# Kernel tuning notes

Hardware: AMD Instinct MI355X
Metric: run time of the kernel (lower is better)

Reference implementation:

```python
import jax, jax.numpy as jnp
import numpy as np

N = 50000      # nodes
E = 800000     # edges
F_IN = 146
D = 256        # repr_len
H = 512        # GENConv hidden (expansion=2)
L = 25         # res blocks
EPS_MSG = 1e-7 # GENConv message eps
T = 0.01       # softmax aggregation temperature


def setup_inputs() -> dict:
    key = jax.random.key(0)
    ks = jax.random.split(key, 8)
    s = lambda k, shape, scale=0.05: jax.random.normal(k, shape, jnp.float32) * scale
    return dict(
        x=jax.random.uniform(ks[0], (N, F_IN), jnp.float32),
        edge_index=jax.random.randint(ks[1], (2, E), 0, N, jnp.int32),
        enc_W=s(ks[2], (F_IN, D)), enc_b=jnp.zeros((D,), jnp.float32),
        conv_W1=s(ks[3], (L, D, H)), conv_b1=jnp.zeros((L, H), jnp.float32),
        conv_ln_g=jnp.ones((L, H), jnp.float32), conv_ln_b=jnp.zeros((L, H), jnp.float32),
        conv_W2=s(ks[4], (L, H, D)), conv_b2=jnp.zeros((L, D), jnp.float32),
        res_ln_g=jnp.ones((L, D), jnp.float32), res_ln_b=jnp.zeros((L, D), jnp.float32),
        fc1_W=s(ks[5], (D, D // 2)), fc1_b=jnp.zeros((D // 2,), jnp.float32),
        out_W=s(ks[6], (D // 2, 1)), out_b=jnp.zeros((1,), jnp.float32),
    )


def layer_norm(x, g, b, eps=1e-5):
    mu = x.mean(-1, keepdims=True)
    var = ((x - mu) ** 2).mean(-1, keepdims=True)
    return (x - mu) * jax.lax.rsqrt(var + eps) * g + b


def genconv(x, src, dst, W1, b1, g1, bb1, W2, b2):
    # message: relu(x_j) + eps  (no edge_attr)
    msg = jax.nn.relu(x[src]) + EPS_MSG                    # [E, D]
    logit = msg * T
    m = jax.ops.segment_max(logit, dst, num_segments=N)    # per-dst, per-feature max
    m = jnp.where(jnp.isfinite(m), m, 0.0)                 # isolated nodes -> 0
    num = jnp.exp(logit - m[dst])
    den = jax.ops.segment_sum(num, dst, num_segments=N)
    alpha = num / (den[dst] + 1e-16)
    agg = jax.ops.segment_sum(alpha * msg, dst, num_segments=N)  # [N, D]
    h = agg + x                                            # root residual inside GENConv
    h = jax.nn.relu(layer_norm(h @ W1 + b1, g1, bb1))      # MLP: Lin->LN->ReLU->Lin
    return h @ W2 + b2


def reference(x, edge_index, enc_W, enc_b, conv_W1, conv_b1, conv_ln_g, conv_ln_b,
              conv_W2, conv_b2, res_ln_g, res_ln_b, fc1_W, fc1_b, out_W, out_b):
    src, dst = edge_index[0], edge_index[1]
    x = x.at[:, 121:].set(x[:, 121:] / 100.0 - 0.5)
    h = x @ enc_W + enc_b
    # layer 0: conv only
    h = genconv(h, src, dst, conv_W1[0], conv_b1[0], conv_ln_g[0], conv_ln_b[0],
                conv_W2[0], conv_b2[0])

    # layers 1..24: res+ block  (dropout=0.1 is identity in eval mode)
    def step(h, p):
        W1, b1, g1, bb1, W2, b2, rg, rb = p
        z = jax.nn.relu(layer_norm(h, rg, rb))
        z = genconv(z, src, dst, W1, b1, g1, bb1, W2, b2)
        return h + z, None

    params = (conv_W1[1:], conv_b1[1:], conv_ln_g[1:], conv_ln_b[1:],
              conv_W2[1:], conv_b2[1:], res_ln_g[1:], res_ln_b[1:])
    h, _ = jax.lax.scan(step, h, params)

    # final: layers[0].act(layers[0].norm(x))
    h = jax.nn.relu(layer_norm(h, res_ln_g[0], res_ln_b[0]))
    h = jax.nn.relu(h @ fc1_W + fc1_b)
    return h @ out_W + out_b
```

## Files before the change

### kernel.cpp

```cpp
#include <hip/hip_runtime.h>

#define NN 50000
#define NE 800000
#define FIN 146
#define DD 256
#define HHD 512
#define NL 25
#define MT 196
#define MT3 782
#define SCAN_NB 49

#define SWZ(r) (((r) >> 1) & 3)

typedef _Float16 h8 __attribute__((ext_vector_type(8)));
typedef float f32x4 __attribute__((ext_vector_type(4)));
typedef unsigned short us8 __attribute__((ext_vector_type(8)));
typedef _Float16 hf4 __attribute__((ext_vector_type(4)));

__device__ __forceinline__ float wsum(float v) {
#pragma unroll
  for (int off = 32; off > 0; off >>= 1) v += __shfl_xor(v, off, 64);
  return v;
}

__device__ __forceinline__ unsigned short f16b(float x) {
  _Float16 h = (_Float16)x;
  return __builtin_bit_cast(unsigned short, h);
}
__device__ __forceinline__ float f16f(unsigned short b) {
  return (float)__builtin_bit_cast(_Float16, b);
}

__device__ __forceinline__ void gl_lds16(const void* g, void* l) {
  __builtin_amdgcn_global_load_lds(
      (const __attribute__((address_space(1))) unsigned int*)g,
      (__attribute__((address_space(3))) unsigned int*)l, 16, 0, 0);
}

__global__ void count_k(const int* __restrict__ ei, int* __restrict__ deg) {
  int e = blockIdx.x * 256 + threadIdx.x;
  if (e < NE) atomicAdd(&deg[ei[NE + e]], 1);
}

__global__ __launch_bounds__(1024) void scan1_k(const int* __restrict__ deg,
                                                int* __restrict__ rp,
                                                int* __restrict__ bsum) {
  __shared__ int buf[1024];
  int tid = threadIdx.x, blk = blockIdx.x;
  int i = blk * 1024 + tid;
  buf[tid] = (i < NN) ? deg[i] : 0;
  __syncthreads();
#pragma unroll
  for (int off = 1; off < 1024; off <<= 1) {
    int t = (tid >= off) ? buf[tid - off] : 0;
    __syncthreads();
    buf[tid] += t;
    __syncthreads();
  }
  if (i < NN) rp[i + 1] = buf[tid];
  if (tid == 1023) bsum[blk] = buf[1023];
}

__global__ void scan2_k(int* __restrict__ bsum) {
  int tid = threadIdx.x;
  int v = (tid < SCAN_NB) ? bsum[tid] : 0;
#pragma unroll
  for (int off = 1; off < 64; off <<= 1) {
    int t = __shfl_up(v, off, 64);
    if (tid >= off) v += t;
  }
  if (tid < SCAN_NB) bsum[tid] = v;
}

__global__ __launch_bounds__(1024) void scan3_k(const int* __restrict__ bsum,
                                                int* __restrict__ rp,
                                                int* __restrict__ deg) {
  int i = blockIdx.x * 1024 + threadIdx.x;
  if (i < NN) {
    int blk = i >> 10;
    if (blk > 0) rp[i + 1] += bsum[blk - 1];
    deg[i] = 0;
  }
  if (i == 0) rp[0] = 0;
}

__global__ void fill_k(const int* __restrict__ ei, const int* __restrict__ rp,
                       int* __restrict__ deg, int* __restrict__ col) {
  int e = blockIdx.x * 256 + threadIdx.x;
  if (e < NE) {
    int d = ei[NE + e];
    int pos = rp[d] + atomicAdd(&deg[d], 1);
    col[pos] = ei[e];
  }
}

__global__ __launch_bounds__(256) void wconv_k(const float* __restrict__ cW1,
                                               const float* __restrict__ cW2,
                                               const float* __restrict__ fcW,
                                               const float* __restrict__ encW,
                                               unsigned short* __restrict__ wbuf,
                                               unsigned short* __restrict__ fc1t,
                                               unsigned short* __restrict__ encT) {
  int z = blockIdx.z;
  const float* W;
  unsigned short* oh;
  int Ksrc, Kpad, N;
  if (z < 50) {
    int l = z >> 1, which = z & 1;
    if (which == 0) { W = cW1 + (size_t)l * 131072; Ksrc = 256; N = 512; oh = wbuf + (size_t)l * 524288; }
    else            { W = cW2 + (size_t)l * 131072; Ksrc = 512; N = 256; oh = wbuf + (size_t)l * 524288 + 262144; }
    Kpad = Ksrc;
  } else if (z == 50) {
    W = fcW; Ksrc = 256; Kpad = 256; N = 128; oh = fc1t;
  } else {
    W = encW; Ksrc = FIN; Kpad = 160; N = 256; oh = encT;
  }
  if ((int)blockIdx.x >= (Kpad >> 5) || (int)blockIdx.y >= (N >> 5)) return;
  __shared__ float tile[32][33];
  int tx = threadIdx.x, ty = threadIdx.y;
  int k0 = blockIdx.x * 32, n0 = blockIdx.y * 32;
#pragma unroll
  for (int i = 0; i < 4; ++i) {
    int r = ty + i * 8;
    int k = k0 + r;
    tile[r][tx] = (k < Ksrc) ? W[(size_t)k * N + n0 + tx] : 0.f;
  }
  __syncthreads();
#pragma unroll
  for (int i = 0; i < 4; ++i) {
    int r = ty + i * 8;
    float v = tile[tx][r];
    oh[(size_t)(n0 + r) * Kpad + k0 + tx] = f16b(v);
  }
}

__global__ __launch_bounds__(256) void agg16_k(const hf4* __restrict__ z16,
                                               const int* __restrict__ rp,
                                               const int* __restrict__ col,
                                               unsigned short* __restrict__ hh16) {
  int node = blockIdx.x * 4 + (threadIdx.x >> 6);
  int lane = threadIdx.x & 63;
  if (node >= NN) return;
  int beg = rp[node], end = rp[node + 1];
  float4 s = make_float4(0.f, 0.f, 0.f, 0.f);
  float4 v = make_float4(0.f, 0.f, 0.f, 0.f);
  int j = beg;
  for (; j + 3 < end; j += 4) {
    int sn0 = col[j], sn1 = col[j + 1], sn2 = col[j + 2], sn3 = col[j + 3];
    hf4 a0 = z16[(size_t)sn0 * 64 + lane];
    hf4 a1 = z16[(size_t)sn1 * 64 + lane];
    hf4 a2 = z16[(size_t)sn2 * 64 + lane];
    hf4 a3 = z16[(size_t)sn3 * 64 + lane];
#pragma unroll
    for (int u = 0; u < 4; ++u) {
      hf4 a = (u == 0) ? a0 : (u == 1) ? a1 : (u == 2) ? a2 : a3;
      float m0 = fmaxf((float)a[0], 0.f) + 1e-7f;
      float m1 = fmaxf((float)a[1], 0.f) + 1e-7f;
      float m2 = fmaxf((float)a[2], 0.f) + 1e-7f;
      float m3 = fmaxf((float)a[3], 0.f) + 1e-7f;
      float e0 = __expf(m0 * 0.01f), e1 = __expf(m1 * 0.01f);
      float e2 = __expf(m2 * 0.01f), e3 = __expf(m3 * 0.01f);
      s.x += e0; s.y += e1; s.z += e2; s.w += e3;
      v.x = fmaf(e0, m0, v.x); v.y = fmaf(e1, m1, v.y);
      v.z = fmaf(e2, m2, v.z); v.w = fmaf(e3, m3, v.w);
    }
  }
  for (; j < end; ++j) {
    int sn = col[j];
    hf4 a = z16[(size_t)sn * 64 + lane];
    float m0 = fmaxf((float)a[0], 0.f) + 1e-7f;
    float m1 = fmaxf((float)a[1], 0.f) + 1e-7f;
    float m2 = fmaxf((float)a[2], 0.f) + 1e-7f;
    float m3 = fmaxf((float)a[3], 0.f) + 1e-7f;
    float e0 = __expf(m0 * 0.01f), e1 = __expf(m1 * 0.01f);
    float e2 = __expf(m2 * 0.01f), e3 = __expf(m3 * 0.01f);
    s.x += e0; s.y += e1; s.z += e2; s.w += e3;
    v.x = fmaf(e0, m0, v.x); v.y = fmaf(e1, m1, v.y);
    v.z = fmaf(e2, m2, v.z); v.w = fmaf(e3, m3, v.w);
  }
  hf4 ow = z16[(size_t)node * 64 + lane];
  float o0 = v.x / (s.x + 1e-16f) + (float)ow[0];
  float o1 = v.y / (s.y + 1e-16f) + (float)ow[1];
  float o2 = v.z / (s.z + 1e-16f) + (float)ow[2];
  float o3 = v.w / (s.w + 1e-16f) + (float)ow[3];
  size_t idx = (size_t)node * DD + lane * 4;
  *(ushort4*)&hh16[idx] = make_ushort4(f16b(o0), f16b(o1), f16b(o2), f16b(o3));
}

template <int AMODE, int ACC, int RELU, int PSUM, int C16, int Z16>
__global__ __launch_bounds__(512, 3) void mgemm_k(
    const float* __restrict__ Af, const unsigned short* __restrict__ A16,
    const unsigned short* __restrict__ BTh,
    const float* __restrict__ bias, float* __restrict__ C, int M, int K, int N,
    int mtiles, int lgnb,
    const float2* __restrict__ stats,
    const float* __restrict__ lng, const float* __restrict__ lnbeta,
    float2* __restrict__ psum_out, unsigned short* __restrict__ z16out) {
  __shared__ __align__(16) unsigned short Ash[2][8192], Bsh[2][4096];
  int tid = threadIdx.x;
  int bi = blockIdx.x;
  int ppx = (mtiles + 7) >> 3;
  int slot = bi >> 3;
  int panel = (bi & 7) * ppx + (slot >> lgnb);
  if (panel >= mtiles) return;
  int nblk = slot & ((1 << lgnb) - 1);
  int bm0 = panel * 256, bn0 = nblk * 128;
  int lane = tid & 63, wv = tid >> 6;
  int wr = (wv >> 1) * 64, wc = (wv & 1) * 64;
  int lr = lane & 15, lc = lane >> 4;
  f32x4 acc[4][4];
  f32x4 zf = {0.f, 0.f, 0.f, 0.f};
#pragma unroll
  for (int mi = 0; mi < 4; ++mi)
#pragma unroll
    for (int ni = 0; ni < 4; ++ni) acc[mi][ni] = zf;

  int sr = tid >> 1, hf = tid & 1;
  int arow = bm0 + sr;

  float mu = 0.f, rstd = 1.f;
  if constexpr (AMODE == 3) {
    if (arow < M) {
      float2 st = stats[arow];
      mu = st.x; rstd = st.y;
    }
  }

  auto stageB = [&](int buf, int k0) {
    int r = tid >> 2, cp = tid & 3;
    int c = cp ^ SWZ(r);
    gl_lds16(BTh + (size_t)(bn0 + r) * K + k0 + c * 8, &Bsh[buf][wv * 512]);
  };
  auto stageA = [&](int buf, int k0) {
    if constexpr (AMODE == 0) {
#pragma unroll
      for (int j = 0; j < 2; ++j) {
        int idx = wv * 128 + j * 64 + lane;
        int r = idx >> 2, cp = idx & 3;
        int c = cp ^ SWZ(r);
        int row = bm0 + r;
        if (row >= M) row = M - 1;
        gl_lds16(A16 + (size_t)row * K + k0 + c * 8, &Ash[buf][wv * 1024 + j * 512]);
      }
    } else {
      float v[16];
      if (arow < M) {
        if constexpr (AMODE == 2) {
          const float* xp = Af + (size_t)arow * FIN;
#pragma unroll
          for (int j = 0; j < 16; ++j) {
            int kk = k0 + hf * 16 + j;
            float t = (kk < FIN) ? xp[kk] : 0.f;
            if (kk >= 121 && kk < FIN) t = t * 0.01f - 0.5f;
            v[j] = t;
          }
        } else {
          const unsigned short* ap = A16 + (size_t)arow * K + k0 + hf * 16;
          us8 p0 = *(const us8*)(ap);
          us8 p1 = *(const us8*)(ap + 8);
          const float* gp = lng + k0 + hf * 16;
          const float* bp = lnbeta + k0 + hf * 16;
#pragma unroll
          for (int j = 0; j < 8; ++j) {
            v[j] = fmaxf(0.f, (f16f(p0[j]) - mu) * rstd * gp[j] + bp[j]);
            v[8 + j] = fmaxf(0.f, (f16f(p1[j]) - mu) * rstd * gp[8 + j] + bp[8 + j]);
          }
        }
      } else {
#pragma unroll
        for (int j = 0; j < 16; ++j) v[j] = 0.f;
      }
      unsigned short hi[16];
#pragma unroll
      for (int j = 0; j < 16; ++j) hi[j] = f16b(v[j]);
      int c0 = hf * 2;
      *(us8*)&Ash[buf][sr * 32 + ((c0 ^ SWZ(sr)) * 8)] = *(us8*)&hi[0];
      *(us8*)&Ash[buf][sr * 32 + (((c0 + 1) ^ SWZ(sr)) * 8)] = *(us8*)&hi[8];
    }
  };

  int nt = K / 32;
  stageA(0, 0);
  stageB(0, 0);
  __syncthreads();
  for (int t = 0; t < nt; ++t) {
    int cur = t & 1;
    h8 a[4], bh[4];
#pragma unroll
    for (int mi = 0; mi < 4; ++mi) {
      int r = wr + mi * 16 + lr;
      a[mi] = *(const h8*)&Ash[cur][r * 32 + ((lc ^ SWZ(r)) * 8)];
    }
#pragma unroll
    for (int ni = 0; ni < 4; ++ni) {
      int n = wc + ni * 16 + lr;
      bh[ni] = *(const h8*)&Bsh[cur][n * 32 + ((lc ^ SWZ(n)) * 8)];
    }
    if (t + 1 < nt) {
      stageA(cur ^ 1, (t + 1) * 32);
      stageB(cur ^ 1, (t + 1) * 32);
    }
    __builtin_amdgcn_s_setprio(1);
#pragma unroll
    for (int mi = 0; mi < 4; ++mi)
#pragma unroll
      for (int ni = 0; ni < 4; ++ni)
        acc[mi][ni] = __builtin_amdgcn_mfma_f32_16x16x32_f16(a[mi], bh[ni], acc[mi][ni], 0, 0, 0);
    __builtin_amdgcn_s_setprio(0);
    __syncthreads();
  }
  float sloc[16], qloc[16];
  if constexpr (PSUM) {
#pragma unroll
    for (int i = 0; i < 16; ++i) { sloc[i] = 0.f; qloc[i] = 0.f; }
  }
#pragma unroll
  for (int ni = 0; ni < 4; ++ni) {
    int colg = bn0 + wc + ni * 16 + lr;
    float bia = bias[colg];
#pragma unroll
    for (int mi = 0; mi < 4; ++mi) {
#pragma unroll
      for (int r = 0; r < 4; ++r) {
        int row = bm0 + wr + mi * 16 + lc * 4 + r;
        if (row < M) {
          float vv = acc[mi][ni][r] + bia;
          if (ACC) vv += C[(size_t)row * N + colg];
          if (RELU) vv = fmaxf(vv, 0.f);
          if constexpr (C16) {
            ((unsigned short*)C)[(size_t)row * N + colg] = f16b(vv);
          } else {
            C[(size_t)row * N + colg] = vv;
          }
          if constexpr (Z16) {
            z16out[(size_t)row * N + colg] = f16b(vv);
          }
          if constexpr (PSUM) {
            sloc[mi * 4 + r] += vv;
            qloc[mi * 4 + r] = fmaf(vv, vv, qloc[mi * 4 + r]);
          }
        }
      }
    }
  }
  if constexpr (PSUM) {
#pragma unroll
    for (int i = 0; i < 16; ++i) {
      float s = sloc[i], q = qloc[i];
#pragma unroll
      for (int off = 1; off < 16; off <<= 1) {
        s += __shfl_xor(s, off, 64);
        q += __shfl_xor(q, off, 64);
      }
      sloc[i] = s; qloc[i] = q;
    }
    __syncthreads();
    float2* lps = (float2*)&Ash[0][0];
    if (wv & 1) {
      if (lr == 0) {
#pragma unroll
        for (int mi = 0; mi < 4; ++mi)
#pragma unroll
          for (int r = 0; r < 4; ++r)
            lps[(wv >> 1) * 64 + mi * 16 + lc * 4 + r] =
                make_float2(sloc[mi * 4 + r], qloc[mi * 4 + r]);
      }
    }
    __syncthreads();
    if (!(wv & 1)) {
      if (lr == 0) {
#pragma unroll
        for (int mi = 0; mi < 4; ++mi)
#pragma unroll
          for (int r = 0; r < 4; ++r) {
            int rl = mi * 16 + lc * 4 + r;
            float2 o = lps[(wv >> 1) * 64 + rl];
            int row = bm0 + wr + rl;
            if (row < M)
              psum_out[(size_t)row * 4 + nblk] =
                  make_float2(sloc[mi * 4 + r] + o.x, qloc[mi * 4 + r] + o.y);
          }
      }
    }
  }
}

template <int ACC, int LAST>
__global__ __launch_bounds__(512, 3) void mgemm2_k(
    const unsigned short* __restrict__ A16,
    const unsigned short* __restrict__ BTh,
    const float* __restrict__ bias, unsigned short* __restrict__ h16,
    const float2* __restrict__ psum_in,
    const float* __restrict__ lng, const float* __restrict__ lnbeta,
    const float* __restrict__ rg, const float* __restrict__ rb,
    unsigned short* __restrict__ z16o, float2* __restrict__ hstats) {
  __shared__ __align__(16) unsigned short Ash[2][2048], Bsh[2][8192];
  const int M = NN, K = HHD, N = DD;
  int tid = threadIdx.x;
  int bi = blockIdx.x;
  int panel = (bi & 7) * 98 + (bi >> 3);
  if (panel >= MT3) return;
  int bm0 = panel * 64;
  int lane = tid & 63, wv = tid >> 6;
  int wr = (wv >> 2) * 32, wc = (wv & 3) * 64;
  int lr = lane & 15, lc = lane >> 4;
  f32x4 acc[2][4];
  f32x4 zf = {0.f, 0.f, 0.f, 0.f};
#pragma unroll
  for (int mi = 0; mi < 2; ++mi)
#pragma unroll
    for (int ni = 0; ni < 4; ++ni) acc[mi][ni] = zf;

  int sr2 = tid >> 2, q = tid & 3;
  int arow = bm0 + sr2;
  float mu = 0.f, rstd = 1.f;
  if (tid < 256 && arow < M) {
    float2 p0 = psum_in[(size_t)arow * 4 + 0];
    float2 p1 = psum_in[(size_t)arow * 4 + 1];
    float2 p2 = psum_in[(size_t)arow * 4 + 2];
    float2 p3 = psum_in[(size_t)arow * 4 + 3];
    float s = p0.x + p1.x + p2.x + p3.x;
    float qq = p0.y + p1.y + p2.y + p3.y;
    mu = s * (1.0f / HHD);
    float var = qq * (1.0f / HHD) - mu * mu;
    rstd = rsqrtf(var + 1e-5f);
  }

  auto stageB = [&](int buf, int k0) {
#pragma unroll
    for (int j = 0; j < 2; ++j) {
      int idx = j * 512 + tid;
      int r = idx >> 2, cp = idx & 3;
      int c = cp ^ SWZ(r);
      gl_lds16(BTh + (size_t)r * K + k0 + c * 8, &Bsh[buf][(j * 512 + wv * 64) * 8]);
    }
  };
  auto stageA = [&](int buf, int k0) {
    if (tid < 256) {
      float v[8];
      if (arow < M) {
        us8 p0 = *(const us8*)(A16 + (size_t)arow * K + k0 + q * 8);
        const float* gp = lng + k0 + q * 8;
        const float* bp = lnbeta + k0 + q * 8;
#pragma unroll
        for (int j = 0; j < 8; ++j)
          v[j] = fmaxf(0.f, (f16f(p0[j]) - mu) * rstd * gp[j] + bp[j]);
      } else {
#pragma unroll
        for (int j = 0; j < 8; ++j) v[j] = 0.f;
      }
      unsigned short hi[8];
#pragma unroll
      for (int j = 0; j < 8; ++j) hi[j] = f16b(v[j]);
      *(us8*)&Ash[buf][sr2 * 32 + ((q ^ SWZ(sr2)) * 8)] = *(us8*)&hi[0];
    }
  };

  const int nt = HHD / 32;
  stageA(0, 0);
  stageB(0, 0);
  __syncthreads();
  for (int t = 0; t < nt; ++t) {
    int cur = t & 1;
    h8 a[2], bh[4];
#pragma unroll
    for (int mi = 0; mi < 2; ++mi) {
      int r = wr + mi * 16 + lr;
      a[mi] = *(const h8*)&Ash[cur][r * 32 + ((lc ^ SWZ(r)) * 8)];
    }
#pragma unroll
    for (int ni = 0; ni < 4; ++ni) {
      int n = wc + ni * 16 + lr;
      bh[ni] = *(const h8*)&Bsh[cur][n * 32 + ((lc ^ SWZ(n)) * 8)];
    }
    if (t + 1 < nt) {
      stageA(cur ^ 1, (t + 1) * 32);
      stageB(cur ^ 1, (t + 1) * 32);
    }
    __builtin_amdgcn_s_setprio(1);
#pragma unroll
    for (int mi = 0; mi < 2; ++mi)
#pragma unroll
      for (int ni = 0; ni < 4; ++ni)
        acc[mi][ni] = __builtin_amdgcn_mfma_f32_16x16x32_f16(a[mi], bh[ni], acc[mi][ni], 0, 0, 0);
    __builtin_amdgcn_s_setprio(0);
    __syncthreads();
  }
  float sloc[8], qloc[8];
#pragma unroll
  for (int i = 0; i < 8; ++i) { sloc[i] = 0.f; qloc[i] = 0.f; }
#pragma unroll
  for (int ni = 0; ni < 4; ++ni) {
    int colg = wc + ni * 16 + lr;
    float bia = bias[colg];
#pragma unroll
    for (int mi = 0; mi < 2; ++mi) {
#pragma unroll
      for (int r = 0; r < 4; ++r) {
        int row = bm0 + wr + mi * 16 + lc * 4 + r;
        float vv = acc[mi][ni][r] + bia;
        if (row < M) {
          if (ACC) vv += f16f(h16[(size_t)row * N + colg]);
          h16[(size_t)row * N + colg] = f16b(vv);
        }
        acc[mi][ni][r] = vv;
        sloc[mi * 4 + r] += vv;
        qloc[mi * 4 + r] = fmaf(vv, vv, qloc[mi * 4 + r]);
      }
    }
  }
#pragma unroll
  for (int i = 0; i < 8; ++i) {
    float s = sloc[i], qq = qloc[i];
#pragma unroll
    for (int off = 1; off < 16; off <<= 1) {
      s += __shfl_xor(s, off, 64);
      qq += __shfl_xor(qq, off, 64);
    }
    sloc[i] = s; qloc[i] = qq;
  }
  __syncthreads();
  float2* lpart = (float2*)&Bsh[0][0];
  float2* rowst = (float2*)&Bsh[1][0];
  if (lr == 0) {
#pragma unroll
    for (int mi = 0; mi < 2; ++mi)
#pragma unroll
      for (int r = 0; r < 4; ++r) {
        int rl = wr + mi * 16 + lc * 4 + r;
        lpart[rl * 4 + (wv & 3)] = make_float2(sloc[mi * 4 + r], qloc[mi * 4 + r]);
      }
  }
  __syncthreads();
  if (tid < 64) {
    float2 p0 = lpart[tid * 4 + 0];
    float2 p1 = lpart[tid * 4 + 1];
    float2 p2 = lpart[tid * 4 + 2];
    float2 p3 = lpart[tid * 4 + 3];
    float s = p0.x + p1.x + p2.x + p3.x;
    float qq = p0.y + p1.y + p2.y + p3.y;
    float m_ = s * (1.0f / DD);
    float var = qq * (1.0f / DD) - m_ * m_;
    float rs = rsqrtf(var + 1e-5f);
    rowst[tid] = make_float2(m_, rs);
    if (LAST) {
      int row = bm0 + tid;
      if (row < M) hstats[row] = make_float2(m_, rs);
    }
  }
  __syncthreads();
  if (!LAST) {
#pragma unroll
    for (int mi = 0; mi < 2; ++mi) {
#pragma unroll
      for (int r = 0; r < 4; ++r) {
        int rl = wr + mi * 16 + lc * 4 + r;
        int row = bm0 + rl;
        if (row < M) {
          float2 st = rowst[rl];
#pragma unroll
          for (int ni = 0; ni < 4; ++ni) {
            int colg = wc + ni * 16 + lr;
            float z = fmaxf(0.f, (acc[mi][ni][r] - st.x) * st.y * rg[colg] + rb[colg]);
            z16o[(size_t)row * N + colg] = f16b(z);
          }
        }
      }
    }
  }
}

__global__ __launch_bounds__(256) void outmv_k(const float* __restrict__ t1,
                                               const float* __restrict__ oW,
                                               const float* __restrict__ ob,
                                               float* __restrict__ out) {
  int row = blockIdx.x * 4 + (threadIdx.x >> 6);
  int lane = threadIdx.x & 63;
  if (row >= NN) return;
  float2 v = *(const float2*)(t1 + (size_t)row * 128 + lane * 2);
  float2 w = *(const float2*)(oW + lane * 2);
  float s = v.x * w.x + v.y * w.y;
  s = wsum(s);
  if (lane == 0) out[row] = s + ob[0];
}

extern "C" void kernel_launch(void* const* d_in, const int* in_sizes, int n_in,
                              void* d_out, int out_size, void* d_ws, size_t ws_size,
                              hipStream_t stream) {
  const float* x = (const float*)d_in[0];
  const int* ei = (const int*)d_in[1];
  const float* encW = (const float*)d_in[2];
  const float* encb = (const float*)d_in[3];
  const float* cW1 = (const float*)d_in[4];
  const float* cb1 = (const float*)d_in[5];
  const float* clg = (const float*)d_in[6];
  const float* clb = (const float*)d_in[7];
  const float* cW2 = (const float*)d_in[8];
  const float* cb2 = (const float*)d_in[9];
  const float* rlg = (const float*)d_in[10];
  const float* rlb = (const float*)d_in[11];
  const float* fcW = (const float*)d_in[12];
  const float* fcb = (const float*)d_in[13];
  const float* oW = (const float*)d_in[14];
  const float* ob = (const float*)d_in[15];
  float* out = (float*)d_out;

  char* w = (char*)d_ws;
  unsigned short* h16 = (unsigned short*)(w);
  unsigned short* mid16 = (unsigned short*)(w + 51200000);
  float* t1 = (float*)(w + 51200000);
  hf4* z16 = (hf4*)(w + 102400000);
  unsigned short* hh16 = (unsigned short*)(w + 128000000);
  float2* psum = (float2*)(w + 153600000);
  float2* hstats = (float2*)(w + 155200000);
  int* rp = (int*)(w + 155600000);
  int* deg = (int*)(w + 155800064);
  int* col = (int*)(w + 156000128);
  unsigned short* wbuf = (unsigned short*)(w + 159200128);
  unsigned short* fc1t = (unsigned short*)(w + 185414528);
  unsigned short* encT = (unsigned short*)(w + 185545600);
  int* bsum = (int*)(w + 185709664);

  hipMemsetAsync(deg, 0, NN * sizeof(int), stream);
  count_k<<<(NE + 255) / 256, 256, 0, stream>>>(ei, deg);
  scan1_k<<<SCAN_NB, 1024, 0, stream>>>(deg, rp, bsum);
  scan2_k<<<1, 64, 0, stream>>>(bsum);
  scan3_k<<<SCAN_NB, 1024, 0, stream>>>(bsum, rp, deg);
  fill_k<<<(NE + 255) / 256, 256, 0, stream>>>(ei, rp, deg, col);

  wconv_k<<<dim3(16, 16, 52), dim3(32, 8), 0, stream>>>(cW1, cW2, fcW, encW, wbuf, fc1t, encT);

  mgemm_k<2, 0, 0, 0, 1, 0><<<400, 512, 0, stream>>>(
      x, nullptr, encT, encb, (float*)h16, NN, 160, DD, MT, 1,
      nullptr, nullptr, nullptr, nullptr, nullptr);

  for (int l = 0; l < NL; ++l) {
    const hf4* zsrc = (l == 0) ? (const hf4*)h16 : z16;
    agg16_k<<<NN / 4, 256, 0, stream>>>(zsrc, rp, col, hh16);

    const unsigned short* w1h = wbuf + (size_t)l * 524288;
    mgemm_k<0, 0, 0, 1, 1, 0><<<800, 512, 0, stream>>>(
        nullptr, hh16, w1h, cb1 + (size_t)l * HHD, (float*)mid16,
        NN, DD, HHD, MT, 2, nullptr, nullptr, nullptr, psum, nullptr);

    const unsigned short* w2h = wbuf + (size_t)l * 524288 + 262144;
    const float* lg = clg + (size_t)l * HHD;
    const float* lb = clb + (size_t)l * HHD;
    if (l == 0) {
      mgemm2_k<0, 0><<<784, 512, 0, stream>>>(
          mid16, w2h, cb2 + (size_t)l * DD, h16, psum, lg, lb,
          rlg + (size_t)(l + 1) * DD, rlb + (size_t)(l + 1) * DD,
          (unsigned short*)z16, nullptr);
    } else if (l < NL - 1) {
      mgemm2_k<1, 0><<<784, 512, 0, stream>>>(
          mid16, w2h, cb2 + (size_t)l * DD, h16, psum, lg, lb,
          rlg + (size_t)(l + 1) * DD, rlb + (size_t)(l + 1) * DD,
          (unsigned short*)z16, nullptr);
    } else {
      mgemm2_k<1, 1><<<784, 512, 0, stream>>>(
          mid16, w2h, cb2 + (size_t)l * DD, h16, psum, lg, lb,
          rlg, rlb, (unsigned short*)z16, hstats);
    }
  }

  mgemm_k<3, 0, 1, 0, 0, 0><<<200, 512, 0, stream>>>(
      nullptr, h16, fc1t, fcb, t1, NN, DD, 128, MT, 0,
      hstats, rlg, rlb, nullptr, nullptr);
  outmv_k<<<NN / 4, 256, 0, stream>>>(t1, oW, ob, out);
}
```

Measured before the change: 4.353 ms.

## Add dedicated 128x128-tile GEMM1 kernel and polynomial exp in aggregation

```diff
diff --git a/kernel.cpp b/kernel.cpp
--- a/kernel.cpp
+++ b/kernel.cpp
@@ -7,6 +7,7 @@
 #define HHD 512
 #define NL 25
 #define MT 196
+#define MT2 391
 #define MT3 782
 #define SCAN_NB 49
 
@@ -29,6 +30,10 @@
 }
 __device__ __forceinline__ float f16f(unsigned short b) {
   return (float)__builtin_bit_cast(_Float16, b);
+}
+
+__device__ __forceinline__ float exp_small(float x) {
+  return fmaf(x, fmaf(x, fmaf(x, 0.16666667f, 0.5f), 1.0f), 1.0f);
 }
 
 __device__ __forceinline__ void gl_lds16(const void* g, void* l) {
@@ -158,8 +163,8 @@
       float m1 = fmaxf((float)a[1], 0.f) + 1e-7f;
       float m2 = fmaxf((float)a[2], 0.f) + 1e-7f;
       float m3 = fmaxf((float)a[3], 0.f) + 1e-7f;
-      float e0 = __expf(m0 * 0.01f), e1 = __expf(m1 * 0.01f);
-      float e2 = __expf(m2 * 0.01f), e3 = __expf(m3 * 0.01f);
+      float e0 = exp_small(m0 * 0.01f), e1 = exp_small(m1 * 0.01f);
+      float e2 = exp_small(m2 * 0.01f), e3 = exp_small(m3 * 0.01f);
       s.x += e0; s.y += e1; s.z += e2; s.w += e3;
       v.x = fmaf(e0, m0, v.x); v.y = fmaf(e1, m1, v.y);
       v.z = fmaf(e2, m2, v.z); v.w = fmaf(e3, m3, v.w);
@@ -172,8 +177,8 @@
     float m1 = fmaxf((float)a[1], 0.f) + 1e-7f;
     float m2 = fmaxf((float)a[2], 0.f) + 1e-7f;
     float m3 = fmaxf((float)a[3], 0.f) + 1e-7f;
-    float e0 = __expf(m0 * 0.01f), e1 = __expf(m1 * 0.01f);
-    float e2 = __expf(m2 * 0.01f), e3 = __expf(m3 * 0.01f);
+    float e0 = exp_small(m0 * 0.01f), e1 = exp_small(m1 * 0.01f);
+    float e2 = exp_small(m2 * 0.01f), e3 = exp_small(m3 * 0.01f);
     s.x += e0; s.y += e1; s.z += e2; s.w += e3;
     v.x = fmaf(e0, m0, v.x); v.y = fmaf(e1, m1, v.y);
     v.z = fmaf(e2, m2, v.z); v.w = fmaf(e3, m3, v.w);
@@ -187,15 +192,136 @@
   *(ushort4*)&hh16[idx] = make_ushort4(f16b(o0), f16b(o1), f16b(o2), f16b(o3));
 }
 
-template <int AMODE, int ACC, int RELU, int PSUM, int C16, int Z16>
+__global__ __launch_bounds__(512, 3) void mgemm1_k(
+    const unsigned short* __restrict__ A16,
+    const unsigned short* __restrict__ BTh,
+    const float* __restrict__ bias, unsigned short* __restrict__ Cout,
+    float2* __restrict__ psum_out) {
+  __shared__ __align__(16) unsigned short Ash[2][4096], Bsh[2][4096];
+  const int M = NN, K = DD, N = HHD;
+  int tid = threadIdx.x;
+  int bi = blockIdx.x;
+  int slot = bi >> 3;
+  int panel = (bi & 7) * 49 + (slot >> 2);
+  if (panel >= MT2) return;
+  int nblk = slot & 3;
+  int bm0 = panel * 128, bn0 = nblk * 128;
+  int lane = tid & 63, wv = tid >> 6;
+  int wr = (wv >> 2) * 64, wc = (wv & 3) * 32;
+  int lr = lane & 15, lc = lane >> 4;
+  f32x4 acc[4][2];
+  f32x4 zf = {0.f, 0.f, 0.f, 0.f};
+#pragma unroll
+  for (int mi = 0; mi < 4; ++mi)
+#pragma unroll
+    for (int ni = 0; ni < 2; ++ni) acc[mi][ni] = zf;
+
+  auto stageA = [&](int buf, int k0) {
+    int r = tid >> 2, cp = tid & 3;
+    int c = cp ^ SWZ(r);
+    int row = bm0 + r;
+    if (row >= M) row = M - 1;
+    gl_lds16(A16 + (size_t)row * K + k0 + c * 8, &Ash[buf][wv * 512]);
+  };
+  auto stageB = [&](int buf, int k0) {
+    int r = tid >> 2, cp = tid & 3;
+    int c = cp ^ SWZ(r);
+    gl_lds16(BTh + (size_t)(bn0 + r) * K + k0 + c * 8, &Bsh[buf][wv * 512]);
+  };
+
+  const int nt = K / 32;
+  stageA(0, 0);
+  stageB(0, 0);
+  __syncthreads();
+  for (int t = 0; t < nt; ++t) {
+    int cur = t & 1;
+    h8 a[4], bh[2];
+#pragma unroll
+    for (int mi = 0; mi < 4; ++mi) {
+      int r = wr + mi * 16 + lr;
+      a[mi] = *(const h8*)&Ash[cur][r * 32 + ((lc ^ SWZ(r)) * 8)];
+    }
+#pragma unroll
+    for (int ni = 0; ni < 2; ++ni) {
+      int n = wc + ni * 16 + lr;
+      bh[ni] = *(const h8*)&Bsh[cur][n * 32 + ((lc ^ SWZ(n)) * 8)];
+    }
+    if (t + 1 < nt) {
+      stageA(cur ^ 1, (t + 1) * 32);
+      stageB(cur ^ 1, (t + 1) * 32);
+    }
+    __builtin_amdgcn_s_setprio(1);
+#pragma unroll
+    for (int mi = 0; mi < 4; ++mi)
+#pragma unroll
+      for (int ni = 0; ni < 2; ++ni)
+        acc[mi][ni] = __builtin_amdgcn_mfma_f32_16x16x32_f16(a[mi], bh[ni], acc[mi][ni], 0, 0, 0);
+    __builtin_amdgcn_s_setprio(0);
+    __syncthreads();
+  }
+  float sloc[16], qloc[16];
+#pragma unroll
+  for (int i = 0; i < 16; ++i) { sloc[i] = 0.f; qloc[i] = 0.f; }
+#pragma unroll
+  for (int ni = 0; ni < 2; ++ni) {
+    int colg = bn0 + wc + ni * 16 + lr;
+    float bia = bias[colg];
+#pragma unroll
+    for (int mi = 0; mi < 4; ++mi) {
+#pragma unroll
+      for (int r = 0; r < 4; ++r) {
+        int row = bm0 + wr + mi * 16 + lc * 4 + r;
+        if (row < M) {
+          float vv = acc[mi][ni][r] + bia;
+          Cout[(size_t)row * N + colg] = f16b(vv);
+          sloc[mi * 4 + r] += vv;
+          qloc[mi * 4 + r] = fmaf(vv, vv, qloc[mi * 4 + r]);
+        }
+      }
+    }
+  }
+#pragma unroll
+  for (int i = 0; i < 16; ++i) {
+    float s = sloc[i], q = qloc[i];
+#pragma unroll
+    for (int off = 1; off < 16; off <<= 1) {
+      s += __shfl_xor(s, off, 64);
+      q += __shfl_xor(q, off, 64);
+    }
+    sloc[i] = s; qloc[i] = q;
+  }
+  __syncthreads();
+  float2* lps = (float2*)&Ash[0][0];
+  if (lr == 0) {
+#pragma unroll
+    for (int mi = 0; mi < 4; ++mi)
+#pragma unroll
+      for (int r = 0; r < 4; ++r) {
+        int rl = wr + mi * 16 + lc * 4 + r;
+        lps[rl * 4 + (wv & 3)] = make_float2(sloc[mi * 4 + r], qloc[mi * 4 + r]);
+      }
+  }
+  __syncthreads();
+  if (tid < 128) {
+    float2 p0 = lps[tid * 4 + 0];
+    float2 p1 = lps[tid * 4 + 1];
+    float2 p2 = lps[tid * 4 + 2];
+    float2 p3 = lps[tid * 4 + 3];
+    int row = bm0 + tid;
+    if (row < M)
+      psum_out[(size_t)row * 4 + nblk] =
+          make_float2(p0.x + p1.x + p2.x + p3.x, p0.y + p1.y + p2.y + p3.y);
+  }
+}
+
+template <int AMODE, int RELU, int C16>
 __global__ __launch_bounds__(512, 3) void mgemm_k(
     const float* __restrict__ Af, const unsigned short* __restrict__ A16,
     const unsigned short* __restrict__ BTh,
     const float* __restrict__ bias, float* __restrict__ C, int M, int K, int N,
     int mtiles, int lgnb,
     const float2* __restrict__ stats,
-    const float* __restrict__ lng, const float* __restrict__ lnbeta,
-    float2* __restrict__ psum_out, unsigned short* __restrict__ z16out) {
+    const float* __restrict__ lng, const float* __restrict__ lnbeta) {
   __shared__ __align__(16) unsigned short Ash[2][8192], Bsh[2][4096];
   int tid = threadIdx.x;
   int bi = blockIdx.x;
@@ -232,51 +358,39 @@
     gl_lds16(BTh + (size_t)(bn0 + r) * K + k0 + c * 8, &Bsh[buf][wv * 512]);
   };
   auto stageA = [&](int buf, int k0) {
-    if constexpr (AMODE == 0) {
-#pragma unroll
-      for (int j = 0; j < 2; ++j) {
-        int idx = wv * 128 + j * 64 + lane;
-        int r = idx >> 2, cp = idx & 3;
-        int c = cp ^ SWZ(r);
-        int row = bm0 + r;
-        if (row >= M) row = M - 1;
-        gl_lds16(A16 + (size_t)row * K + k0 + c * 8, &Ash[buf][wv * 1024 + j * 512]);
+    float v[16];
+    if (arow < M) {
+      if constexpr (AMODE == 2) {
+        const float* xp = Af + (size_t)arow * FIN;
+#pragma unroll
+        for (int j = 0; j < 16; ++j) {
+          int kk = k0 + hf * 16 + j;
+          float t = (kk < FIN) ? xp[kk] : 0.f;
+          if (kk >= 121 && kk < FIN) t = t * 0.01f - 0.5f;
+          v[j] = t;
+        }
+      } else {
+        const unsigned short* ap = A16 + (size_t)arow * K + k0 + hf * 16;
+        us8 p0 = *(const us8*)(ap);
+        us8 p1 = *(const us8*)(ap + 8);
+        const float* gp = lng + k0 + hf * 16;
+        const float* bp = lnbeta + k0 + hf * 16;
+#pragma unroll
+        for (int j = 0; j < 8; ++j) {
+          v[j] = fmaxf(0.f, (f16f(p0[j]) - mu) * rstd * gp[j] + bp[j]);
+          v[8 + j] = fmaxf(0.f, (f16f(p1[j]) - mu) * rstd * gp[8 + j] + bp[8 + j]);
+        }
       }
     } else {
-      float v[16];
-      if (arow < M) {
-        if constexpr (AMODE == 2) {
-          const float* xp = Af + (size_t)arow * FIN;
-#pragma unroll
-          for (int j = 0; j < 16; ++j) {
-            int kk = k0 + hf * 16 + j;
-            float t = (kk < FIN) ? xp[kk] : 0.f;
-            if (kk >= 121 && kk < FIN) t = t * 0.01f - 0.5f;
-            v[j] = t;
-          }
-        } else {
-          const unsigned short* ap = A16 + (size_t)arow * K + k0 + hf * 16;
-          us8 p0 = *(const us8*)(ap);
-          us8 p1 = *(const us8*)(ap + 8);
-          const float* gp = lng + k0 + hf * 16;
-          const float* bp = lnbeta + k0 + hf * 16;
-#pragma unroll
-          for (int j = 0; j < 8; ++j) {
-            v[j] = fmaxf(0.f, (f16f(p0[j]) - mu) * rstd * gp[j] + bp[j]);
-            v[8 + j] = fmaxf(0.f, (f16f(p1[j]) - mu) * rstd * gp[8 + j] + bp[8 + j]);
-          }
-        }
-      } else {
-#pragma unroll
-        for (int j = 0; j < 16; ++j) v[j] = 0.f;
-      }
-      unsigned short hi[16];
-#pragma unroll
-      for (int j = 0; j < 16; ++j) hi[j] = f16b(v[j]);
-      int c0 = hf * 2;
-      *(us8*)&Ash[buf][sr * 32 + ((c0 ^ SWZ(sr)) * 8)] = *(us8*)&hi[0];
-      *(us8*)&Ash[buf][sr * 32 + (((c0 + 1) ^ SWZ(sr)) * 8)] = *(us8*)&hi[8];
-    }
+#pragma unroll
+      for (int j = 0; j < 16; ++j) v[j] = 0.f;
+    }
+    unsigned short hi[16];
+#pragma unroll
+    for (int j = 0; j < 16; ++j) hi[j] = f16b(v[j]);
+    int c0 = hf * 2;
+    *(us8*)&Ash[buf][sr * 32 + ((c0 ^ SWZ(sr)) * 8)] = *(us8*)&hi[0];
+    *(us8*)&Ash[buf][sr * 32 + (((c0 + 1) ^ SWZ(sr)) * 8)] = *(us8*)&hi[8];
   };
 
   int nt = K / 32;
@@ -309,11 +423,6 @@
     __builtin_amdgcn_s_setprio(0);
     __syncthreads();
   }
-  float sloc[16], qloc[16];
-  if constexpr (PSUM) {
-#pragma unroll
-    for (int i = 0; i < 16; ++i) { sloc[i] = 0.f; qloc[i] = 0.f; }
-  }
 #pragma unroll
   for (int ni = 0; ni < 4; ++ni) {
     int colg = bn0 + wc + ni * 16 + lr;
@@ -325,61 +434,13 @@
         int row = bm0 + wr + mi * 16 + lc * 4 + r;
         if (row < M) {
           float vv = acc[mi][ni][r] + bia;
-          if (ACC) vv += C[(size_t)row * N + colg];
           if (RELU) vv = fmaxf(vv, 0.f);
           if constexpr (C16) {
             ((unsigned short*)C)[(size_t)row * N + colg] = f16b(vv);
           } else {
             C[(size_t)row * N + colg] = vv;
           }
-          if constexpr (Z16) {
-            z16out[(size_t)row * N + colg] = f16b(vv);
-          }
-          if constexpr (PSUM) {
-            sloc[mi * 4 + r] += vv;
-            qloc[mi * 4 + r] = fmaf(vv, vv, qloc[mi * 4 + r]);
-          }
         }
-      }
-    }
-  }
-  if constexpr (PSUM) {
-#pragma unroll
-    for (int i = 0; i < 16; ++i) {
-      float s = sloc[i], q = qloc[i];
-#pragma unroll
-      for (int off = 1; off < 16; off <<= 1) {
-        s += __shfl_xor(s, off, 64);
-        q += __shfl_xor(q, off, 64);
-      }
-      sloc[i] = s; qloc[i] = q;
-    }
-    __syncthreads();
-    float2* lps = (float2*)&Ash[0][0];
-    if (wv & 1) {
-      if (lr == 0) {
-#pragma unroll
-        for (int mi = 0; mi < 4; ++mi)
-#pragma unroll
-          for (int r = 0; r < 4; ++r)
-            lps[(wv >> 1) * 64 + mi * 16 + lc * 4 + r] =
-                make_float2(sloc[mi * 4 + r], qloc[mi * 4 + r]);
-      }
-    }
-    __syncthreads();
-    if (!(wv & 1)) {
-      if (lr == 0) {
-#pragma unroll
-        for (int mi = 0; mi < 4; ++mi)
-#pragma unroll
-          for (int r = 0; r < 4; ++r) {
-            int rl = mi * 16 + lc * 4 + r;
-            float2 o = lps[(wv >> 1) * 64 + rl];
-            int row = bm0 + wr + rl;
-            if (row < M)
-              psum_out[(size_t)row * 4 + nblk] =
-                  make_float2(sloc[mi * 4 + r] + o.x, qloc[mi * 4 + r] + o.y);
-          }
       }
     }
   }
@@ -630,18 +691,17 @@
 
   wconv_k<<<dim3(16, 16, 52), dim3(32, 8), 0, stream>>>(cW1, cW2, fcW, encW, wbuf, fc1t, encT);
 
-  mgemm_k<2, 0, 0, 0, 1, 0><<<400, 512, 0, stream>>>(
+  mgemm_k<2, 0, 1><<<400, 512, 0, stream>>>(
       x, nullptr, encT, encb, (float*)h16, NN, 160, DD, MT, 1,
-      nullptr, nullptr, nullptr, nullptr, nullptr);
+      nullptr, nullptr, nullptr);
 
   for (int l = 0; l < NL; ++l) {
     const hf4* zsrc = (l == 0) ? (const hf4*)h16 : z16;
     agg16_k<<<NN / 4, 256, 0, stream>>>(zsrc, rp, col, hh16);
 
     const unsigned short* w1h = wbuf + (size_t)l * 524288;
-    mgemm_k<0, 0, 0, 1, 1, 0><<<800, 512, 0, stream>>>(
-        nullptr, hh16, w1h, cb1 + (size_t)l * HHD, (float*)mid16,
-        NN, DD, HHD, MT, 2, nullptr, nullptr, nullptr, psum, nullptr);
+    mgemm1_k<<<1568, 512, 0, stream>>>(
+        hh16, w1h, cb1 + (size_t)l * HHD, mid16, psum);
 
     const unsigned short* w2h = wbuf + (size_t)l * 524288 + 262144;
     const float* lg = clg + (size_t)l * HHD;
@@ -663,8 +723,8 @@
     }
   }
 
-  mgemm_k<3, 0, 1, 0, 0, 0><<<200, 512, 0, stream>>>(
+  mgemm_k<3, 1, 0><<<200, 512, 0, stream>>>(
       nullptr, h16, fc1t, fcb, t1, NN, DD, 128, MT, 0,
-      hstats, rlg, rlb, nullptr, nullptr);
+      hstats, rlg, rlb);
   outmv_k<<<NN / 4, 256, 0, stream>>>(t1, oW, ob, out);
 }
```

After: 4.386 ms. Within noise of the previous version (+0.8%).
